# Optimization experiments

Hardware: AMD Instinct MI355X
Metric: run time of the kernel (lower is better)

Reference implementation:

```python
import jax, jax.numpy as jnp
import numpy as np
from jax import lax

LN_EPS = 1e-5

D_MODEL, N_HEADS, HEAD_DIM, RANK, POWER_K = 1024, 16, 64, 32, 4
RIDGE_EPS, SPECTRAL_GAMMA = 1e-4, 0.99


def setup_inputs() -> dict:
    key = jax.random.key(0)
    ks = jax.random.split(key, 8)
    B, T = 4, 4096
    s = 1.0 / np.sqrt(D_MODEL)
    inp = {
        "hidden_states": jax.random.normal(ks[0], (B, T, D_MODEL), dtype=jnp.float32),
        "Wk": jax.random.normal(ks[1], (D_MODEL, N_HEADS * RANK), dtype=jnp.float32) * s,
        "Wq": jax.random.normal(ks[2], (D_MODEL, N_HEADS * RANK), dtype=jnp.float32) * s,
        "Wv": jax.random.normal(ks[3], (D_MODEL, N_HEADS * HEAD_DIM), dtype=jnp.float32) * s,
        "Wo": jax.random.normal(ks[4], (N_HEADS * HEAD_DIM, D_MODEL), dtype=jnp.float32) * s,
        "ln_scale": jnp.ones((D_MODEL,), jnp.float32),
        "ln_bias": jnp.zeros((D_MODEL,), jnp.float32),
        "gate_alpha": jnp.zeros((1,), jnp.float32),
        "log_ridge": jnp.array(np.log(RIDGE_EPS), jnp.float32),
        "log_gamma": jnp.array(np.log(SPECTRAL_GAMMA), jnp.float32),
        "prefix_len": 2048,
    }
    return inp


def _tri_solve(L, b, transpose=False):
    # solves L x = b (or L^T x = b) with lower-triangular L; batched over leading dims
    return lax.linalg.triangular_solve(L, b, left_side=True, lower=True, transpose_a=transpose)


def _build_operator(keys, values, ridge, gamma):
    # keys: (B,H,L,r), values: (B,H,L,dh)
    r = keys.shape[-1]
    G = jnp.einsum('bhlr,bhls->bhrs', keys, keys) + ridge * jnp.eye(r, dtype=keys.dtype)
    M = jnp.einsum('bhlr,bhls->bhrs', keys[:, :, 1:, :], keys[:, :, :-1, :])
    L = jnp.linalg.cholesky(G)                       # (B,H,r,r)
    U = _tri_solve(L, M)                             # L^{-1} M
    V = _tri_solve(L, jnp.swapaxes(U, -1, -2))       # L^{-1} (L^{-1}M)^T
    A_w = jnp.swapaxes(V, -1, -2)                    # L^{-1} M L^{-T}
    gamma_c = jnp.minimum(gamma, 1.0)
    sigma = jnp.linalg.svd(A_w, compute_uv=False)[..., 0]  # spectral norm
    sigma = jnp.maximum(sigma, 1e-8)
    scale = gamma_c / jnp.maximum(sigma, 1.0)
    A_w = A_w * scale[..., None, None]
    C_v = jnp.einsum('bhld,bhlr->bhdr', values, keys)       # (B,H,dh,r)
    Y = _tri_solve(L, jnp.swapaxes(C_v, -1, -2))            # L^{-1} C_v^T
    Bv_T = _tri_solve(L, Y, transpose=True)                 # G^{-1} C_v^T
    B_v = jnp.swapaxes(Bv_T, -1, -2)                        # (B,H,dh,r)
    return A_w, L, B_v


def _spectral_filter(A_w, L, B_v, queries, power_K):
    # queries: (B,H,Q,r) -> (B,H,Q,dh)
    qT = jnp.swapaxes(queries, -1, -2)      # (B,H,r,Q)
    w = _tri_solve(L, qT)                   # whiten
    for _ in range(power_K):
        w = jnp.matmul(A_w, w)
    z_hat = jnp.matmul(L, w)                # unwhiten
    out = jnp.matmul(B_v, z_hat)            # (B,H,dh,Q)
    return jnp.swapaxes(out, -1, -2)


def reference(hidden_states, Wk, Wq, Wv, Wo, ln_scale, ln_bias,
              gate_alpha, log_ridge, log_gamma, prefix_len):
    B, T, D = hidden_states.shape
    P = max(1, min(int(prefix_len), T - 1))
    mu = jnp.mean(hidden_states, axis=-1, keepdims=True)
    var = jnp.var(hidden_states, axis=-1, keepdims=True)
    normed = (hidden_states - mu) / jnp.sqrt(var + LN_EPS) * ln_scale + ln_bias
    def proj(W, dim):
        y = normed @ W
        return jnp.swapaxes(y.reshape(B, T, N_HEADS, dim), 1, 2)  # (B,H,T,dim)
    keys_all = proj(Wk, RANK)
    queries_all = proj(Wq, RANK)
    values_all = proj(Wv, HEAD_DIM)
    ridge = jnp.exp(log_ridge)
    gamma = jnp.exp(log_gamma)
    A_w, L, B_v = _build_operator(keys_all[:, :, :P, :], values_all[:, :, :P, :], ridge, gamma)
    q_out = _spectral_filter(A_w, L, B_v, queries_all[:, :, P:, :], POWER_K)
    p_out = _spectral_filter(A_w, L, B_v, keys_all[:, :, :P, :], POWER_K)
    full = jnp.concatenate([p_out, q_out], axis=2)               # (B,H,T,dh)
    full = jnp.swapaxes(full, 1, 2).reshape(B, T, N_HEADS * HEAD_DIM)
    out = full @ Wo
    return jax.nn.sigmoid(gate_alpha) * out
```

## Files before the change

### kernel.cpp

```cpp
#include <hip/hip_runtime.h>
#include <math.h>

#define D_MODEL 1024
#define TT 4096
#define NB 4
#define NH 16
#define TCH 8

typedef __attribute__((ext_vector_type(8))) short s8v;
typedef __attribute__((ext_vector_type(4))) float f4v;
typedef __attribute__((ext_vector_type(8))) unsigned short u16x8;

#define OFF_STATS ((size_t)0)
#define OFF_GP    ((size_t)(1) << 20)
#define OFF_MP    ((size_t)(3) << 20)
#define OFF_CP    ((size_t)(5) << 20)
#define OFF_FT    ((size_t)(9) << 20)
#define OFF_WKH   ((size_t)(10) << 20)
#define OFF_WKL   ((size_t)(11) << 20)
#define OFF_WQH   ((size_t)(12) << 20)
#define OFF_WQL   ((size_t)(13) << 20)
#define OFF_WVH   ((size_t)(14) << 20)
#define OFF_WVL   ((size_t)(16) << 20)
#define OFF_WOH   ((size_t)(18) << 20)
#define OFF_WOL   ((size_t)(20) << 20)
#define OFF_Y1    ((size_t)(22) << 20)
#define OFF_Y2    ((size_t)(54) << 20)
#define OFF_FH    OFF_Y2

__device__ __forceinline__ unsigned short bf16_rne(float x) {
  unsigned u = __float_as_uint(x);
  return (unsigned short)((u + 0x7fffu + ((u >> 16) & 1u)) >> 16);
}
__device__ __forceinline__ void split_bf16(float x, unsigned short& h, unsigned short& l) {
  unsigned u = __float_as_uint(x);
  unsigned r = (u + 0x7fffu + ((u >> 16) & 1u)) & 0xffff0000u;
  h = (unsigned short)(r >> 16);
  float res = x - __uint_as_float(r);
  l = bf16_rne(res);
}

__device__ __forceinline__ void gll16(unsigned short* lds, const unsigned short* g) {
  __builtin_amdgcn_global_load_lds(
      (__attribute__((address_space(1))) void*)(void*)(g),
      (__attribute__((address_space(3))) void*)(lds), 16, 0, 0);
}

__device__ __forceinline__ void xcd_swz(int gx, int gy, int& x, int& y, int& z) {
  int wg = blockIdx.x + gx * (blockIdx.y + gy * blockIdx.z);
  int k = wg & 7, j = wg >> 3;
  x = j % gx;
  int yz = k + ((j / gx) << 3);
  y = yz % gy;
  z = yz / gy;
}

__global__ __launch_bounds__(256) void ln_stats_k(const float* __restrict__ X,
                                                  float* __restrict__ stats) {
  int r = blockIdx.x;
  const float4 v = ((const float4*)(X + (size_t)r * D_MODEL))[threadIdx.x];
  float s  = v.x + v.y + v.z + v.w;
  float ss = v.x * v.x + v.y * v.y + v.z * v.z + v.w * v.w;
#pragma unroll
  for (int off = 32; off > 0; off >>= 1) {
    s  += __shfl_down(s, off, 64);
    ss += __shfl_down(ss, off, 64);
  }
  __shared__ float as_[4], bs_[4];
  int w = threadIdx.x >> 6, lane = threadIdx.x & 63;
  if (lane == 0) { as_[w] = s; bs_[w] = ss; }
  __syncthreads();
  if (threadIdx.x == 0) {
    float S  = as_[0] + as_[1] + as_[2] + as_[3];
    float SS = bs_[0] + bs_[1] + bs_[2] + bs_[3];
    float mu  = S * (1.0f / D_MODEL);
    float var = SS * (1.0f / D_MODEL) - mu * mu;
    stats[2 * (size_t)r]     = mu;
    stats[2 * (size_t)r + 1] = 1.0f / sqrtf(var + 1e-5f);
  }
}

__global__ __launch_bounds__(256) void prep_w_k(const float* __restrict__ W, int N,
                                                unsigned short* __restrict__ Thi,
                                                unsigned short* __restrict__ Tlo,
                                                int swz) {
  __shared__ float tileT[32 * 33];
  const int n0 = blockIdx.x * 32, k0 = blockIdx.y * 32;
  const int tid = threadIdx.x;
  {
    int k_l = tid >> 3, n4 = (tid & 7) << 2;
    float4 v = *(const float4*)&W[(size_t)(k0 + k_l) * N + n0 + n4];
    tileT[(n4 + 0) * 33 + k_l] = v.x;
    tileT[(n4 + 1) * 33 + k_l] = v.y;
    tileT[(n4 + 2) * 33 + k_l] = v.z;
    tileT[(n4 + 3) * 33 + k_l] = v.w;
  }
  __syncthreads();
  {
    int n_l = tid >> 3, k4 = (tid & 7) << 2;
    unsigned short h[4], l[4];
#pragma unroll
    for (int i = 0; i < 4; i++) split_bf16(tileT[n_l * 33 + k4 + i], h[i], l[i]);
    int kc = k0 + k4;
    int col = kc;
    if (swz == 1)
      col = (kc & ~63) | ((((kc >> 3) & 7) ^ (n_l & 7)) << 3) | (kc & 7);
    else if (swz == 2)
      col = (kc & ~31) | ((((kc >> 3) & 3) ^ ((n_l >> 1) & 3)) << 3) | (kc & 7);
    *(ushort4*)&Thi[(size_t)(n0 + n_l) * 1024 + col] = make_ushort4(h[0], h[1], h[2], h[3]);
    *(ushort4*)&Tlo[(size_t)(n0 + n_l) * 1024 + col] = make_ushort4(l[0], l[1], l[2], l[3]);
  }
}

__global__ __launch_bounds__(512) void gemm_ln_k(
    const float* __restrict__ X, const float* __restrict__ stats,
    const float* __restrict__ lng, const float* __restrict__ lnb,
    const unsigned short* __restrict__ BH0, const unsigned short* __restrict__ BL0,
    const unsigned short* __restrict__ BH1, const unsigned short* __restrict__ BL1,
    const int* __restrict__ pref, int mode, int Nw, float* __restrict__ Y) {
  int P = pref[0]; P = P < 1 ? 1 : (P > TT - 1 ? TT - 1 : P);
  int xx, yy, zz;
  xcd_swz(gridDim.x, 32, xx, yy, zz);
  const int b  = zz;
  const int t0 = yy * 128;
  const int n0 = xx * 256;
  if (mode == 2 && t0 >= P) return;
  const int row0 = b * TT + t0;
  const bool hasK = (t0 < P);
  const bool hasQ = (t0 + 128 > P);

  __shared__ __align__(16) unsigned short aH[2 * 128 * 40], aL[2 * 128 * 40];
  __shared__ __align__(16) unsigned short bH[2 * 256 * 32], bL[2 * 256 * 32];
  __shared__ float lngs[1024], lnbs[1024];

  const int tid = threadIdx.x;
  const int lane = tid & 63;
  const int wid  = tid >> 6;
  const int wm = (wid >> 2) * 64, wn = (wid & 3) * 64;
  const int lm = lane & 15, lq = lane >> 4;
  const int arow = tid >> 2, acol = (tid & 3) << 3;
  const int l4 = lane >> 2, c4 = (lane & 3) << 3;

  for (int e = tid; e < 1024; e += 512) { lngs[e] = lng[e]; lnbs[e] = lnb[e]; }
  const float mu = stats[2 * (size_t)(row0 + arow)];
  const float rs = stats[2 * (size_t)(row0 + arow) + 1];

  for (int pass = 0; pass < 2; ++pass) {
    if (mode == 2) { if (pass == 1) break; }
    else { if (pass == 0 && !hasK) continue; if (pass == 1 && !hasQ) continue; }
    const unsigned short* WH = pass ? BH1 : BH0;
    const unsigned short* WL = pass ? BL1 : BL0;

    f4v acc[4][4];
#pragma unroll
    for (int i = 0; i < 4; i++)
#pragma unroll
      for (int j = 0; j < 4; j++) acc[i][j] = (f4v){0.f, 0.f, 0.f, 0.f};

    float4 xE[2], xO[2];

    auto XLOAD = [&](int t, float4 (&xr)[2]) {
      const float* src = &X[(size_t)(row0 + arow) * 1024 + t * 32 + acol];
      xr[0] = *(const float4*)src;
      xr[1] = *(const float4*)(src + 4);
    };
    auto STAGEB = [&](int t, int buf) {
      const int kt = t * 32;
#pragma unroll
      for (int i = 0; i < 2; i++) {
        int iss = wid * 2 + i;
        int r = n0 + iss * 16 + l4;
        gll16(&bH[buf * 8192 + iss * 512], &WH[(size_t)r * 1024 + kt + c4]);
        gll16(&bL[buf * 8192 + iss * 512], &WL[(size_t)r * 1024 + kt + c4]);
      }
    };
    auto LNW = [&](int tt, float4 (&xr)[2], int abuf) {
      const int kt = tt * 32;
      float4 lg0 = *(const float4*)&lngs[kt + acol];
      float4 lg1 = *(const float4*)&lngs[kt + acol + 4];
      float4 lb0 = *(const float4*)&lnbs[kt + acol];
      float4 lb1 = *(const float4*)&lnbs[kt + acol + 4];
      float xv[8] = {xr[0].x, xr[0].y, xr[0].z, xr[0].w,
                     xr[1].x, xr[1].y, xr[1].z, xr[1].w};
      float lgv[8] = {lg0.x, lg0.y, lg0.z, lg0.w, lg1.x, lg1.y, lg1.z, lg1.w};
      float lbv[8] = {lb0.x, lb0.y, lb0.z, lb0.w, lb1.x, lb1.y, lb1.z, lb1.w};
      u16x8 hv, lv;
#pragma unroll
      for (int i = 0; i < 8; i++) {
        float nv = (xv[i] - mu) * rs * lgv[i] + lbv[i];
        unsigned short h, l;
        split_bf16(nv, h, l);
        hv[i] = h; lv[i] = l;
      }
      int ao = abuf * 5120 + arow * 40 + acol;
      *(u16x8*)&aH[ao] = hv;
      *(u16x8*)&aL[ao] = lv;
    };

    auto ITER = [&](int t, float4 (&xrd)[2], float4 (&xwr)[2]) {
      const int buf = t & 1;
      asm volatile("s_waitcnt vmcnt(6)" ::: "memory");
      __builtin_amdgcn_s_barrier();
      s8v ah[4], al[4], bh[4], bl[4];
#pragma unroll
      for (int i = 0; i < 4; i++) {
        int rA = wm + i * 16 + lm;
        int rB = wn + i * 16 + lm;
        int ao = buf * 5120 + rA * 40 + lq * 8;
        int bo = buf * 8192 + rB * 32 + ((lq ^ ((rB >> 1) & 3)) << 3);
        ah[i] = *(const s8v*)&aH[ao];
        al[i] = *(const s8v*)&aL[ao];
        bh[i] = *(const s8v*)&bH[bo];
        bl[i] = *(const s8v*)&bL[bo];
      }
      __builtin_amdgcn_s_setprio(1);
#pragma unroll
      for (int mi = 0; mi < 4; mi++)
#pragma unroll
        for (int ni = 0; ni < 4; ni++) {
          acc[mi][ni] = __builtin_amdgcn_mfma_f32_16x16x32_bf16(ah[mi], bh[ni], acc[mi][ni], 0, 0, 0);
          acc[mi][ni] = __builtin_amdgcn_mfma_f32_16x16x32_bf16(ah[mi], bl[ni], acc[mi][ni], 0, 0, 0);
          acc[mi][ni] = __builtin_amdgcn_mfma_f32_16x16x32_bf16(al[mi], bh[ni], acc[mi][ni], 0, 0, 0);
        }
      __builtin_amdgcn_s_setprio(0);
      if (t < 31) LNW(t + 1, xrd, buf ^ 1);
      asm volatile("s_waitcnt lgkmcnt(0)" ::: "memory");
      __builtin_amdgcn_s_barrier();
      if (t < 30) {
        XLOAD(t + 2, xwr);
        STAGEB(t + 2, buf);
      }
    };

    XLOAD(0, xE); STAGEB(0, 0);
    XLOAD(1, xO); STAGEB(1, 1);
    __syncthreads();
    LNW(0, xE, 0);
    __syncthreads();

    for (int t2 = 0; t2 < 32; t2 += 2) {
      ITER(t2,     xO, xE);
      ITER(t2 + 1, xE, xO);
    }

#pragma unroll
    for (int mi = 0; mi < 4; mi++) {
#pragma unroll
      for (int r = 0; r < 4; r++) {
        int t = t0 + wm + mi * 16 + lq * 4 + r;
        bool ok = (mode == 2) ? (t < P) : (pass ? (t >= P) : (t < P));
        if (!ok) continue;
        size_t orow = (mode == 2) ? ((size_t)b * P + t) : ((size_t)b * TT + t);
#pragma unroll
        for (int ni = 0; ni < 4; ni++)
          Y[orow * Nw + n0 + wn + ni * 16 + lm] = acc[mi][ni][r];
      }
    }
  }
}

__global__ __launch_bounds__(256) void build_gmc_mfma_k(
    const float* __restrict__ Y1, const float* __restrict__ Y2,
    const int* __restrict__ pref,
    float* __restrict__ Gp, float* __restrict__ Mp, float* __restrict__ Cp) {
  int P = pref[0]; P = P < 1 ? 1 : (P > TT - 1 ? TT - 1 : P);
  const int c  = blockIdx.x;
  const int bh = blockIdx.y;
  const int b = bh >> 4, h = bh & 15;
  const int chunk = (P + TCH - 1) / TCH;
  const int tb = c * chunk;
  const int te = min(tb + chunk, P);

  __shared__ __align__(16) unsigned short kCh[32 * 136], kCl[32 * 136];
  __shared__ __align__(16) unsigned short kPh[32 * 136], kPl[32 * 136];
  __shared__ __align__(16) unsigned short vTh[64 * 136], vTl[64 * 136];

  const int tid = threadIdx.x;
  const int wid = tid >> 6, lane = tid & 63;
  const int lm = lane & 15, lq = lane >> 4;

  f4v acc[4];
#pragma unroll
  for (int i = 0; i < 4; i++) acc[i] = (f4v){0.f, 0.f, 0.f, 0.f};

  for (int t0 = tb; t0 < te; t0 += 128) {
    const int len = (te - t0 < 128) ? (te - t0) : 128;
    __syncthreads();
    for (int e = tid; e < 129 * 8; e += 256) {
      int row = e >> 3, j4 = (e & 7) << 2;
      int t = t0 - 1 + row;
      float4 kv = make_float4(0.f, 0.f, 0.f, 0.f);
      if (row <= len && t >= 0)
        kv = *(const float4*)&Y1[((size_t)b * TT + t) * 512 + h * 32 + j4];
      unsigned short hh[4], ll[4];
      split_bf16(kv.x, hh[0], ll[0]); split_bf16(kv.y, hh[1], ll[1]);
      split_bf16(kv.z, hh[2], ll[2]); split_bf16(kv.w, hh[3], ll[3]);
      if (row >= 1) {
#pragma unroll
        for (int q = 0; q < 4; q++) {
          kCh[(j4 + q) * 136 + row - 1] = hh[q];
          kCl[(j4 + q) * 136 + row - 1] = ll[q];
        }
      }
      if (row < 128) {
#pragma unroll
        for (int q = 0; q < 4; q++) {
          kPh[(j4 + q) * 136 + row] = hh[q];
          kPl[(j4 + q) * 136 + row] = ll[q];
        }
      }
    }
    for (int e = tid; e < 128 * 16; e += 256) {
      int row = e >> 4, dj = (e & 15) << 2;
      int t = t0 + row;
      float4 vv = make_float4(0.f, 0.f, 0.f, 0.f);
      if (row < len)
        vv = *(const float4*)&Y2[((size_t)b * P + t) * 1024 + h * 64 + dj];
      unsigned short hh[4], ll[4];
      split_bf16(vv.x, hh[0], ll[0]); split_bf16(vv.y, hh[1], ll[1]);
      split_bf16(vv.z, hh[2], ll[2]); split_bf16(vv.w, hh[3], ll[3]);
#pragma unroll
      for (int q = 0; q < 4; q++) {
        vTh[(dj + q) * 136 + row] = hh[q];
        vTl[(dj + q) * 136 + row] = ll[q];
      }
    }
    __syncthreads();

#pragma unroll
    for (int kk = 0; kk < 128; kk += 32) {
      const int off = kk + lq * 8;
      if (wid == 0) {
        s8v h0 = *(const s8v*)&kCh[(0 + lm) * 136 + off];
        s8v h1 = *(const s8v*)&kCh[(16 + lm) * 136 + off];
        s8v l0 = *(const s8v*)&kCl[(0 + lm) * 136 + off];
        s8v l1 = *(const s8v*)&kCl[(16 + lm) * 136 + off];
        acc[0] = __builtin_amdgcn_mfma_f32_16x16x32_bf16(h0, h0, acc[0], 0, 0, 0);
        acc[0] = __builtin_amdgcn_mfma_f32_16x16x32_bf16(h0, l0, acc[0], 0, 0, 0);
        acc[0] = __builtin_amdgcn_mfma_f32_16x16x32_bf16(l0, h0, acc[0], 0, 0, 0);
        acc[1] = __builtin_amdgcn_mfma_f32_16x16x32_bf16(h0, h1, acc[1], 0, 0, 0);
        acc[1] = __builtin_amdgcn_mfma_f32_16x16x32_bf16(h0, l1, acc[1], 0, 0, 0);
        acc[1] = __builtin_amdgcn_mfma_f32_16x16x32_bf16(l0, h1, acc[1], 0, 0, 0);
        acc[2] = __builtin_amdgcn_mfma_f32_16x16x32_bf16(h1, h0, acc[2], 0, 0, 0);
        acc[2] = __builtin_amdgcn_mfma_f32_16x16x32_bf16(h1, l0, acc[2], 0, 0, 0);
        acc[2] = __builtin_amdgcn_mfma_f32_16x16x32_bf16(l1, h0, acc[2], 0, 0, 0);
        acc[3] = __builtin_amdgcn_mfma_f32_16x16x32_bf16(h1, h1, acc[3], 0, 0, 0);
        acc[3] = __builtin_amdgcn_mfma_f32_16x16x32_bf16(h1, l1, acc[3], 0, 0, 0);
        acc[3] = __builtin_amdgcn_mfma_f32_16x16x32_bf16(l1, h1, acc[3], 0, 0, 0);
      } else if (wid == 1) {
        s8v ah0 = *(const s8v*)&kCh[(0 + lm) * 136 + off];
        s8v ah1 = *(const s8v*)&kCh[(16 + lm) * 136 + off];
        s8v al0 = *(const s8v*)&kCl[(0 + lm) * 136 + off];
        s8v al1 = *(const s8v*)&kCl[(16 + lm) * 136 + off];
        s8v bh0 = *(const s8v*)&kPh[(0 + lm) * 136 + off];
        s8v bh1 = *(const s8v*)&kPh[(16 + lm) * 136 + off];
        s8v bl0 = *(const s8v*)&kPl[(0 + lm) * 136 + off];
        s8v bl1 = *(const s8v*)&kPl[(16 + lm) * 136 + off];
        acc[0] = __builtin_amdgcn_mfma_f32_16x16x32_bf16(ah0, bh0, acc[0], 0, 0, 0);
        acc[0] = __builtin_amdgcn_mfma_f32_16x16x32_bf16(ah0, bl0, acc[0], 0, 0, 0);
        acc[0] = __builtin_amdgcn_mfma_f32_16x16x32_bf16(al0, bh0, acc[0], 0, 0, 0);
        acc[1] = __builtin_amdgcn_mfma_f32_16x16x32_bf16(ah0, bh1, acc[1], 0, 0, 0);
        acc[1] = __builtin_amdgcn_mfma_f32_16x16x32_bf16(ah0, bl1, acc[1], 0, 0, 0);
        acc[1] = __builtin_amdgcn_mfma_f32_16x16x32_bf16(al0, bh1, acc[1], 0, 0, 0);
        acc[2] = __builtin_amdgcn_mfma_f32_16x16x32_bf16(ah1, bh0, acc[2], 0, 0, 0);
        acc[2] = __builtin_amdgcn_mfma_f32_16x16x32_bf16(ah1, bl0, acc[2], 0, 0, 0);
        acc[2] = __builtin_amdgcn_mfma_f32_16x16x32_bf16(al1, bh0, acc[2], 0, 0, 0);
        acc[3] = __builtin_amdgcn_mfma_f32_16x16x32_bf16(ah1, bh1, acc[3], 0, 0, 0);
        acc[3] = __builtin_amdgcn_mfma_f32_16x16x32_bf16(ah1, bl1, acc[3], 0, 0, 0);
        acc[3] = __builtin_amdgcn_mfma_f32_16x16x32_bf16(al1, bh1, acc[3], 0, 0, 0);
      } else {
        const int d0 = (wid - 2) * 32;
        s8v vh0 = *(const s8v*)&vTh[(d0 + lm) * 136 + off];
        s8v vh1 = *(const s8v*)&vTh[(d0 + 16 + lm) * 136 + off];
        s8v vl0 = *(const s8v*)&vTl[(d0 + lm) * 136 + off];
        s8v vl1 = *(const s8v*)&vTl[(d0 + 16 + lm) * 136 + off];
        s8v kh0 = *(const s8v*)&kCh[(0 + lm) * 136 + off];
        s8v kh1 = *(const s8v*)&kCh[(16 + lm) * 136 + off];
        s8v kl0 = *(const s8v*)&kCl[(0 + lm) * 136 + off];
        s8v kl1 = *(const s8v*)&kCl[(16 + lm) * 136 + off];
        acc[0] = __builtin_amdgcn_mfma_f32_16x16x32_bf16(vh0, kh0, acc[0], 0, 0, 0);
        acc[0] = __builtin_amdgcn_mfma_f32_16x16x32_bf16(vh0, kl0, acc[0], 0, 0, 0);
        acc[0] = __builtin_amdgcn_mfma_f32_16x16x32_bf16(vl0, kh0, acc[0], 0, 0, 0);
        acc[1] = __builtin_amdgcn_mfma_f32_16x16x32_bf16(vh0, kh1, acc[1], 0, 0, 0);
        acc[1] = __builtin_amdgcn_mfma_f32_16x16x32_bf16(vh0, kl1, acc[1], 0, 0, 0);
        acc[1] = __builtin_amdgcn_mfma_f32_16x16x32_bf16(vl0, kh1, acc[1], 0, 0, 0);
        acc[2] = __builtin_amdgcn_mfma_f32_16x16x32_bf16(vh1, kh0, acc[2], 0, 0, 0);
        acc[2] = __builtin_amdgcn_mfma_f32_16x16x32_bf16(vh1, kl0, acc[2], 0, 0, 0);
        acc[2] = __builtin_amdgcn_mfma_f32_16x16x32_bf16(vl1, kh0, acc[2], 0, 0, 0);
        acc[3] = __builtin_amdgcn_mfma_f32_16x16x32_bf16(vh1, kh1, acc[3], 0, 0, 0);
        acc[3] = __builtin_amdgcn_mfma_f32_16x16x32_bf16(vh1, kl1, acc[3], 0, 0, 0);
        acc[3] = __builtin_amdgcn_mfma_f32_16x16x32_bf16(vl1, kh1, acc[3], 0, 0, 0);
      }
    }
  }

  if (wid < 2) {
    float* dst = (wid == 0 ? Gp : Mp) + (size_t)(c * 64 + bh) * 1024;
#pragma unroll
    for (int t = 0; t < 4; t++) {
      int i0 = (t >> 1) * 16, j0 = (t & 1) * 16;
#pragma unroll
      for (int r = 0; r < 4; r++)
        dst[(i0 + lq * 4 + r) * 32 + j0 + lm] = acc[t][r];
    }
  } else {
    float* dst = Cp + (size_t)(c * 64 + bh) * 2048;
#pragma unroll
    for (int t = 0; t < 4; t++) {
      int d0 = (wid - 2) * 32 + (t >> 1) * 16, j0 = (t & 1) * 16;
#pragma unroll
      for (int r = 0; r < 4; r++)
        dst[(d0 + lq * 4 + r) * 32 + j0 + lm] = acc[t][r];
    }
  }
}

__global__ __launch_bounds__(256) void solve_op_k(
    const float* __restrict__ Gp, const float* __restrict__ Mp,
    const float* __restrict__ Cp, const float* __restrict__ lridge,
    const float* __restrict__ lgamma, float* __restrict__ Ft) {
  __shared__ float Gs[32 * 33];
  __shared__ float Ms[32 * 32];
  __shared__ float Gi[32 * 32];
  __shared__ float W2s[32 * 33];
  __shared__ float Aw[32 * 33];
  __shared__ float Nn[32 * 32];
  __shared__ float N2[32 * 32];
  __shared__ float T1[32 * 32];
  __shared__ float Cs[64 * 32];
  __shared__ float red[256];
  const int bh = blockIdx.x;
  const int tid = threadIdx.x;
  const float ridge = expf(lridge[0]);

  for (int e = tid; e < 1024; e += 256) {
    int i = e >> 5, j = e & 31;
    float g = 0.f, m = 0.f;
#pragma unroll
    for (int cc = 0; cc < TCH; cc++) {
      g += Gp[(size_t)(cc * 64 + bh) * 1024 + e];
      m += Mp[(size_t)(cc * 64 + bh) * 1024 + e];
    }
    if (i == j) g += ridge;
    Gs[i * 33 + j] = g;
    Ms[e] = m;
  }
  for (int e = tid; e < 2048; e += 256) {
    float s = 0.f;
#pragma unroll
    for (int cc = 0; cc < TCH; cc++) s += Cp[(size_t)(cc * 64 + bh) * 2048 + e];
    Cs[e] = s;
  }
  __syncthreads();

  for (int j = 0; j < 32; j++) {
    float d = Gs[j * 33 + j];
    __syncthreads();
    float inv = 1.0f / sqrtf(d);
    if (tid >= j && tid < 32) Gs[tid * 33 + j] *= inv;
    __syncthreads();
    int w = 31 - j;
    for (int e = tid; e < w * w; e += 256) {
      int i = j + 1 + e / w, k = j + 1 + e % w;
      Gs[i * 33 + k] -= Gs[i * 33 + j] * Gs[k * 33 + j];
    }
    __syncthreads();
  }

  if (tid < 32) {
    const int c = tid;
    float w[32];
#pragma unroll
    for (int i = 0; i < 32; i++) {
      float s = (i == c) ? 1.0f : 0.0f;
#pragma unroll
      for (int j = 0; j < 32; j++)
        if (j < i) s -= Gs[i * 33 + j] * w[j];
      w[i] = s / Gs[i * 33 + i];
    }
#pragma unroll
    for (int i = 31; i >= 0; i--) {
      float s = w[i];
#pragma unroll
      for (int j = 0; j < 32; j++)
        if (j > i) s -= Gs[j * 33 + i] * w[j];
      w[i] = s / Gs[i * 33 + i];
    }
#pragma unroll
    for (int i = 0; i < 32; i++) Gi[i * 32 + c] = w[i];
  } else if (tid >= 64 && tid < 96) {
    const int c = tid - 64;
    float w[32];
#pragma unroll
    for (int i = 0; i < 32; i++) {
      float s = Ms[i * 32 + c];
#pragma unroll
      for (int j = 0; j < 32; j++)
        if (j < i) s -= Gs[i * 33 + j] * w[j];
      w[i] = s / Gs[i * 33 + i];
    }
#pragma unroll
    for (int i = 0; i < 32; i++) W2s[i * 33 + c] = w[i];
  }
  __syncthreads();
  if (tid < 32) {
    const int c = tid;
    float a[32];
#pragma unroll
    for (int i = 0; i < 32; i++) {
      float s = W2s[c * 33 + i];
#pragma unroll
      for (int j = 0; j < 32; j++)
        if (j < i) s -= Gs[i * 33 + j] * a[j];
      a[i] = s / Gs[i * 33 + i];
    }
#pragma unroll
    for (int i = 0; i < 32; i++) Aw[i * 33 + c] = a[i];
  }
  __syncthreads();

  float s0 = 0.0f;
  for (int e = tid; e < 1024; e += 256) {
    float a = Aw[(e >> 5) * 33 + (e & 31)];
    s0 += a * a;
  }
  red[tid] = s0;
  __syncthreads();
  for (int off = 128; off > 0; off >>= 1) {
    if (tid < off) red[tid] += red[tid + off];
    __syncthreads();
  }
  float frob2 = red[0];
  float sigma;
  if (frob2 <= 1.0f) {
    sigma = sqrtf(frob2);
  } else {
    if (tid < 32) {
      const int i = tid;
      float v = 1.0f + 0.001f * (float)i;
      float sig = 0.0f, prev = -1.0f;
      for (int it = 0; it < 64; it++) {
        float u = 0.0f;
#pragma unroll
        for (int j = 0; j < 32; j++) u += Aw[i * 33 + j] * __shfl(v, j, 64);
        float n2 = u * u;
#pragma unroll
        for (int o = 16; o > 0; o >>= 1) n2 += __shfl_xor(n2, o, 64);
        u /= fmaxf(sqrtf(n2), 1e-30f);
        float vn = 0.0f;
#pragma unroll
        for (int j = 0; j < 32; j++) vn += Aw[j * 33 + i] * __shfl(u, j, 64);
        float m2 = vn * vn;
#pragma unroll
        for (int o = 16; o > 0; o >>= 1) m2 += __shfl_xor(m2, o, 64);
        sig = sqrtf(m2);
        v = vn / fmaxf(sig, 1e-30f);
        if (it >= 7 && fabsf(sig - prev) <= 1e-7f * sig) break;
        prev = sig;
      }
      if (i == 0) red[0] = sig;
    }
    __syncthreads();
    sigma = red[0];
  }
  float gamma_c = fminf(expf(lgamma[0]), 1.0f);
  float scale = gamma_c / fmaxf(fmaxf(sigma, 1e-8f), 1.0f);

  for (int e = tid; e < 1024; e += 256) {
    int i = e >> 5, c = e & 31;
    float s = 0;
#pragma unroll
    for (int k = 0; k < 32; k++) s += Ms[i * 32 + k] * Gi[k * 32 + c];
    Nn[e] = scale * s;
  }
  __syncthreads();
  for (int e = tid; e < 1024; e += 256) {
    int i = e >> 5, c = e & 31;
    float s = 0;
#pragma unroll
    for (int k = 0; k < 32; k++) s += Nn[i * 32 + k] * Nn[k * 32 + c];
    N2[e] = s;
  }
  __syncthreads();
  for (int e = tid; e < 1024; e += 256) {
    int i = e >> 5, c = e & 31;
    float s = 0;
#pragma unroll
    for (int k = 0; k < 32; k++) s += N2[i * 32 + k] * N2[k * 32 + c];
    Ms[e] = s;
  }
  __syncthreads();
  for (int e = tid; e < 1024; e += 256) {
    int i = e >> 5, c = e & 31;
    float s = 0;
#pragma unroll
    for (int k = 0; k < 32; k++) s += Gi[i * 32 + k] * Ms[k * 32 + c];
    T1[e] = s;
  }
  __syncthreads();
  for (int e = tid; e < 2048; e += 256) {
    int j = e >> 6, d = e & 63;
    float s = 0;
#pragma unroll
    for (int k = 0; k < 32; k++) s += Cs[d * 32 + k] * T1[k * 32 + j];
    Ft[(size_t)bh * 2048 + e] = s;
  }
}

__global__ __launch_bounds__(256) void apply_k(const float* __restrict__ Y1,
                                               const float* __restrict__ Ft,
                                               unsigned short* __restrict__ FH) {
  __shared__ float xs[128 * 32];
  const int h = blockIdx.y;
  const int r0 = blockIdx.x * 128;
  const int bh = (r0 >> 12) * NH + h;
  const int tid = threadIdx.x;
  const int d = tid & 63, t0 = tid >> 6;
  float fcol[32];
  const float* fb = &Ft[(size_t)bh * 2048 + d];
#pragma unroll
  for (int j = 0; j < 32; j++) fcol[j] = fb[j * 64];
  for (int e = tid; e < 1024; e += 256) {
    int row = e >> 3, j4 = (e & 7) << 2;
    *(float4*)&xs[row * 32 + j4] =
        *(const float4*)&Y1[((size_t)(r0 + row)) * 512 + h * 32 + j4];
  }
  __syncthreads();
  const int dq = d >> 3, dr = d & 7;
  for (int tl = t0; tl < 128; tl += 4) {
    float s = 0;
#pragma unroll
    for (int j = 0; j < 32; j++) s += xs[tl * 32 + j] * fcol[j];
    int col = h * 64 + ((dq ^ (tl & 7)) << 3) + dr;
    FH[((size_t)(r0 + tl)) * 1024 + col] = bf16_rne(s);
  }
}

__global__ __launch_bounds__(512) void gemm_out_k(
    const unsigned short* __restrict__ FH,
    const unsigned short* __restrict__ WThi, const unsigned short* __restrict__ WTlo,
    const float* __restrict__ alpha, float* __restrict__ out) {
  __shared__ __align__(16) unsigned short lds[65536];
  int xx, yy, zz;
  xcd_swz(8, 64, xx, yy, zz);
  const int m0 = yy * 256;
  const int n0 = xx * 128;
  const int tid = threadIdx.x;
  const int lane = tid & 63;
  const int wid  = tid >> 6;
  const int wm = (wid >> 1) * 64;
  const int wn = (wid & 1) * 64;
  const int lm = lane & 15, lq = lane >> 4;
  const int l8 = lane >> 3, c8 = (lane & 7) << 3;

  f4v acc[4][4];
#pragma unroll
  for (int i = 0; i < 4; i++)
#pragma unroll
    for (int j = 0; j < 4; j++) acc[i][j] = (f4v){0.f, 0.f, 0.f, 0.f};

  auto STAGE = [&](int t, int buf) {
    const int kt = t * 64;
#pragma unroll
    for (int i = 0; i < 4; i++) {
      int iss = wid * 4 + i;
      gll16(&lds[buf * 16384 + iss * 512],
            &FH[(size_t)(m0 + iss * 8 + l8) * 1024 + kt + c8]);
    }
#pragma unroll
    for (int i = 0; i < 2; i++) {
      int iss = wid * 2 + i;
      gll16(&lds[32768 + buf * 8192 + iss * 512],
            &WThi[(size_t)(n0 + iss * 8 + l8) * 1024 + kt + c8]);
    }
#pragma unroll
    for (int i = 0; i < 2; i++) {
      int iss = wid * 2 + i;
      gll16(&lds[49152 + buf * 8192 + iss * 512],
            &WTlo[(size_t)(n0 + iss * 8 + l8) * 1024 + kt + c8]);
    }
  };

  STAGE(0, 0);
  STAGE(1, 1);

  for (int t = 0; t < 16; t++) {
    const int buf = t & 1;
    if (t < 15) asm volatile("s_waitcnt vmcnt(8)" ::: "memory");
    else        asm volatile("s_waitcnt vmcnt(0)" ::: "memory");
    __builtin_amdgcn_s_barrier();
    const unsigned short* Ab  = &lds[buf * 16384];
    const unsigned short* Bhb = &lds[32768 + buf * 8192];
    const unsigned short* Blb = &lds[49152 + buf * 8192];
    __builtin_amdgcn_s_setprio(1);
#pragma unroll
    for (int kk = 0; kk < 2; kk++) {
      s8v ah[4], bh[4], bl[4];
#pragma unroll
      for (int i = 0; i < 4; i++) {
        int rA = wm + i * 16 + lm;
        int rB = wn + i * 16 + lm;
        int sA = (((kk * 4 + lq) ^ (rA & 7)) << 3);
        int sB = (((kk * 4 + lq) ^ (rB & 7)) << 3);
        ah[i] = *(const s8v*)&Ab[rA * 64 + sA];
        bh[i] = *(const s8v*)&Bhb[rB * 64 + sB];
        bl[i] = *(const s8v*)&Blb[rB * 64 + sB];
      }
#pragma unroll
      for (int mi = 0; mi < 4; mi++)
#pragma unroll
        for (int ni = 0; ni < 4; ni++) {
          acc[mi][ni] = __builtin_amdgcn_mfma_f32_16x16x32_bf16(ah[mi], bh[ni], acc[mi][ni], 0, 0, 0);
          acc[mi][ni] = __builtin_amdgcn_mfma_f32_16x16x32_bf16(ah[mi], bl[ni], acc[mi][ni], 0, 0, 0);
        }
    }
    __builtin_amdgcn_s_setprio(0);
    __builtin_amdgcn_sched_barrier(0);
    __builtin_amdgcn_s_barrier();
    if (t < 14) STAGE(t + 2, buf);
  }

  float sg = 1.0f / (1.0f + expf(-alpha[0]));
#pragma unroll
  for (int mi = 0; mi < 4; mi++)
#pragma unroll
    for (int r = 0; r < 4; r++) {
      size_t orow = (size_t)(m0 + wm + mi * 16 + lq * 4 + r);
#pragma unroll
      for (int ni = 0; ni < 4; ni++)
        out[orow * 1024 + n0 + wn + ni * 16 + lm] = sg * acc[mi][ni][r];
    }
}

extern "C" void kernel_launch(void* const* d_in, const int* in_sizes, int n_in,
                              void* d_out, int out_size, void* d_ws, size_t ws_size,
                              hipStream_t stream) {
  const float* X      = (const float*)d_in[0];
  const float* Wk     = (const float*)d_in[1];
  const float* Wq     = (const float*)d_in[2];
  const float* Wv     = (const float*)d_in[3];
  const float* Wo     = (const float*)d_in[4];
  const float* lng    = (const float*)d_in[5];
  const float* lnb    = (const float*)d_in[6];
  const float* alpha  = (const float*)d_in[7];
  const float* lridge = (const float*)d_in[8];
  const float* lgamma = (const float*)d_in[9];
  const int*   pref   = (const int*)d_in[10];
  float* out = (float*)d_out;
  char* ws = (char*)d_ws;
  float* stats = (float*)(ws + OFF_STATS);
  float* Gp    = (float*)(ws + OFF_GP);
  float* Mp    = (float*)(ws + OFF_MP);
  float* Cp    = (float*)(ws + OFF_CP);
  float* Ft    = (float*)(ws + OFF_FT);
  unsigned short* WKH = (unsigned short*)(ws + OFF_WKH);
  unsigned short* WKL = (unsigned short*)(ws + OFF_WKL);
  unsigned short* WQH = (unsigned short*)(ws + OFF_WQH);
  unsigned short* WQL = (unsigned short*)(ws + OFF_WQL);
  unsigned short* WVH = (unsigned short*)(ws + OFF_WVH);
  unsigned short* WVL = (unsigned short*)(ws + OFF_WVL);
  unsigned short* WOH = (unsigned short*)(ws + OFF_WOH);
  unsigned short* WOL = (unsigned short*)(ws + OFF_WOL);
  float* Y1 = (float*)(ws + OFF_Y1);
  float* Y2 = (float*)(ws + OFF_Y2);
  unsigned short* FH = (unsigned short*)(ws + OFF_FH);

  ln_stats_k<<<16384, 256, 0, stream>>>(X, stats);
  prep_w_k<<<dim3(16, 32), 256, 0, stream>>>(Wk, 512, WKH, WKL, 2);
  prep_w_k<<<dim3(16, 32), 256, 0, stream>>>(Wq, 512, WQH, WQL, 2);
  prep_w_k<<<dim3(32, 32), 256, 0, stream>>>(Wv, 1024, WVH, WVL, 2);
  prep_w_k<<<dim3(32, 32), 256, 0, stream>>>(Wo, 1024, WOH, WOL, 1);
  gemm_ln_k<<<dim3(2, 32, NB), 512, 0, stream>>>(X, stats, lng, lnb,
      WKH, WKL, WQH, WQL, pref, 0, 512, Y1);
  gemm_ln_k<<<dim3(4, 32, NB), 512, 0, stream>>>(X, stats, lng, lnb,
      WVH, WVL, WVH, WVL, pref, 2, 1024, Y2);
  build_gmc_mfma_k<<<dim3(TCH, 64), 256, 0, stream>>>(Y1, Y2, pref, Gp, Mp, Cp);
  solve_op_k<<<64, 256, 0, stream>>>(Gp, Mp, Cp, lridge, lgamma, Ft);
  apply_k<<<dim3(128, NH), 256, 0, stream>>>(Y1, Ft, FH);
  gemm_out_k<<<dim3(8, 64), 512, 0, stream>>>(FH, WOH, WOL, alpha, out);
}
```

Measured before the change: 418.9 us.

## Restructure output GEMM into 4-slot K=32 pipeline with 32-wide swizzle

The output projection GEMM moves from a double-buffered K=64 tile loop to a four-slot ring of K=32 stages, issuing loads three stages ahead and syncing once per stage. The FH and Wo staging layouts change to a 32-column XOR swizzle to match the narrower tile, and the apply kernel and Wo prep are updated to write that layout. The aim is to hide global-load latency better and cut barrier stalls. In exchange it adds more loop iterations and waitcnt points, and every LDS read now waits on lgkmcnt(0) before the MFMAs.

```diff
diff --git a/kernel.cpp b/kernel.cpp
--- a/kernel.cpp
+++ b/kernel.cpp
@@ -103,9 +103,7 @@
     for (int i = 0; i < 4; i++) split_bf16(tileT[n_l * 33 + k4 + i], h[i], l[i]);
     int kc = k0 + k4;
     int col = kc;
-    if (swz == 1)
-      col = (kc & ~63) | ((((kc >> 3) & 7) ^ (n_l & 7)) << 3) | (kc & 7);
-    else if (swz == 2)
+    if (swz == 2)
       col = (kc & ~31) | ((((kc >> 3) & 3) ^ ((n_l >> 1) & 3)) << 3) | (kc & 7);
     *(ushort4*)&Thi[(size_t)(n0 + n_l) * 1024 + col] = make_ushort4(h[0], h[1], h[2], h[3]);
     *(ushort4*)&Tlo[(size_t)(n0 + n_l) * 1024 + col] = make_ushort4(l[0], l[1], l[2], l[3]);
@@ -626,12 +624,12 @@
         *(const float4*)&Y1[((size_t)(r0 + row)) * 512 + h * 32 + j4];
   }
   __syncthreads();
-  const int dq = d >> 3, dr = d & 7;
+  const int dq2 = (d >> 3) & 3, dhi = d & 32, dr = d & 7;
   for (int tl = t0; tl < 128; tl += 4) {
     float s = 0;
 #pragma unroll
     for (int j = 0; j < 32; j++) s += xs[tl * 32 + j] * fcol[j];
-    int col = h * 64 + ((dq ^ (tl & 7)) << 3) + dr;
+    int col = h * 64 + dhi + ((dq2 ^ ((tl >> 1) & 3)) << 3) + dr;
     FH[((size_t)(r0 + tl)) * 1024 + col] = bf16_rne(s);
   }
 }
@@ -651,7 +649,7 @@
   const int wm = (wid >> 1) * 64;
   const int wn = (wid & 1) * 64;
   const int lm = lane & 15, lq = lane >> 4;
-  const int l8 = lane >> 3, c8 = (lane & 7) << 3;
+  const int l4 = lane >> 2, c4 = (lane & 3) << 3;
 
   f4v acc[4][4];
 #pragma unroll
@@ -659,65 +657,52 @@
 #pragma unroll
     for (int j = 0; j < 4; j++) acc[i][j] = (f4v){0.f, 0.f, 0.f, 0.f};
 
-  auto STAGE = [&](int t, int buf) {
-    const int kt = t * 64;
-#pragma unroll
-    for (int i = 0; i < 4; i++) {
-      int iss = wid * 4 + i;
-      gll16(&lds[buf * 16384 + iss * 512],
-            &FH[(size_t)(m0 + iss * 8 + l8) * 1024 + kt + c8]);
-    }
+  auto STAGE = [&](int s) {
+    const int slot = s & 3;
+    const int kt = s * 32;
 #pragma unroll
     for (int i = 0; i < 2; i++) {
       int iss = wid * 2 + i;
-      gll16(&lds[32768 + buf * 8192 + iss * 512],
-            &WThi[(size_t)(n0 + iss * 8 + l8) * 1024 + kt + c8]);
-    }
-#pragma unroll
-    for (int i = 0; i < 2; i++) {
-      int iss = wid * 2 + i;
-      gll16(&lds[49152 + buf * 8192 + iss * 512],
-            &WTlo[(size_t)(n0 + iss * 8 + l8) * 1024 + kt + c8]);
-    }
+      gll16(&lds[slot * 8192 + iss * 512],
+            &FH[(size_t)(m0 + iss * 16 + l4) * 1024 + kt + c4]);
+    }
+    gll16(&lds[32768 + slot * 4096 + wid * 512],
+          &WThi[(size_t)(n0 + wid * 16 + l4) * 1024 + kt + c4]);
+    gll16(&lds[49152 + slot * 4096 + wid * 512],
+          &WTlo[(size_t)(n0 + wid * 16 + l4) * 1024 + kt + c4]);
   };
 
-  STAGE(0, 0);
-  STAGE(1, 1);
-
-  for (int t = 0; t < 16; t++) {
-    const int buf = t & 1;
-    if (t < 15) asm volatile("s_waitcnt vmcnt(8)" ::: "memory");
-    else        asm volatile("s_waitcnt vmcnt(0)" ::: "memory");
+  STAGE(0); STAGE(1); STAGE(2);
+  asm volatile("s_waitcnt vmcnt(8)" ::: "memory");
+  __builtin_amdgcn_s_barrier();
+
+  for (int s = 0; s < 32; s++) {
+    const int slot = s & 3;
+    if (s < 29) STAGE(s + 3);
+    s8v ah[4], bh[4], bl[4];
+#pragma unroll
+    for (int i = 0; i < 4; i++) {
+      int rA = wm + i * 16 + lm;
+      int rB = wn + i * 16 + lm;
+      ah[i] = *(const s8v*)&lds[slot * 8192 + rA * 32 + ((lq ^ ((rA >> 1) & 3)) << 3)];
+      bh[i] = *(const s8v*)&lds[32768 + slot * 4096 + rB * 32 + ((lq ^ ((rB >> 1) & 3)) << 3)];
+      bl[i] = *(const s8v*)&lds[49152 + slot * 4096 + rB * 32 + ((lq ^ ((rB >> 1) & 3)) << 3)];
+    }
+    if (s < 29)       asm volatile("s_waitcnt vmcnt(8)" ::: "memory");
+    else if (s == 29) asm volatile("s_waitcnt vmcnt(4)" ::: "memory");
+    else if (s == 30) asm volatile("s_waitcnt vmcnt(0)" ::: "memory");
+    asm volatile("s_waitcnt lgkmcnt(0)" ::: "memory");
+    __builtin_amdgcn_sched_barrier(0);
+    __builtin_amdgcn_s_setprio(1);
+#pragma unroll
+    for (int mi = 0; mi < 4; mi++)
+#pragma unroll
+      for (int ni = 0; ni < 4; ni++) {
+        acc[mi][ni] = __builtin_amdgcn_mfma_f32_16x16x32_bf16(ah[mi], bh[ni], acc[mi][ni], 0, 0, 0);
+        acc[mi][ni] = __builtin_amdgcn_mfma_f32_16x16x32_bf16(ah[mi], bl[ni], acc[mi][ni], 0, 0, 0);
+      }
+    __builtin_amdgcn_s_setprio(0);
     __builtin_amdgcn_s_barrier();
-    const unsigned short* Ab  = &lds[buf * 16384];
-    const unsigned short* Bhb = &lds[32768 + buf * 8192];
-    const unsigned short* Blb = &lds[49152 + buf * 8192];
-    __builtin_amdgcn_s_setprio(1);
-#pragma unroll
-    for (int kk = 0; kk < 2; kk++) {
-      s8v ah[4], bh[4], bl[4];
-#pragma unroll
-      for (int i = 0; i < 4; i++) {
-        int rA = wm + i * 16 + lm;
-        int rB = wn + i * 16 + lm;
-        int sA = (((kk * 4 + lq) ^ (rA & 7)) << 3);
-        int sB = (((kk * 4 + lq) ^ (rB & 7)) << 3);
-        ah[i] = *(const s8v*)&Ab[rA * 64 + sA];
-        bh[i] = *(const s8v*)&Bhb[rB * 64 + sB];
-        bl[i] = *(const s8v*)&Blb[rB * 64 + sB];
-      }
-#pragma unroll
-      for (int mi = 0; mi < 4; mi++)
-#pragma unroll
-        for (int ni = 0; ni < 4; ni++) {
-          acc[mi][ni] = __builtin_amdgcn_mfma_f32_16x16x32_bf16(ah[mi], bh[ni], acc[mi][ni], 0, 0, 0);
-          acc[mi][ni] = __builtin_amdgcn_mfma_f32_16x16x32_bf16(ah[mi], bl[ni], acc[mi][ni], 0, 0, 0);
-        }
-    }
-    __builtin_amdgcn_s_setprio(0);
-    __builtin_amdgcn_sched_barrier(0);
-    __builtin_amdgcn_s_barrier();
-    if (t < 14) STAGE(t + 2, buf);
   }
 
   float sg = 1.0f / (1.0f + expf(-alpha[0]));
@@ -769,7 +754,7 @@
   prep_w_k<<<dim3(16, 32), 256, 0, stream>>>(Wk, 512, WKH, WKL, 2);
   prep_w_k<<<dim3(16, 32), 256, 0, stream>>>(Wq, 512, WQH, WQL, 2);
   prep_w_k<<<dim3(32, 32), 256, 0, stream>>>(Wv, 1024, WVH, WVL, 2);
-  prep_w_k<<<dim3(32, 32), 256, 0, stream>>>(Wo, 1024, WOH, WOL, 1);
+  prep_w_k<<<dim3(32, 32), 256, 0, stream>>>(Wo, 1024, WOH, WOL, 2);
   gemm_ln_k<<<dim3(2, 32, NB), 512, 0, stream>>>(X, stats, lng, lnb,
       WKH, WKL, WQH, WQL, pref, 0, 512, Y1);
   gemm_ln_k<<<dim3(4, 32, NB), 512, 0, stream>>>(X, stats, lng, lnb,
```

New measurement: 415.1 us. About the same (-0.9%).
